# Kernel optimization log

Measured on AMD Instinct MI355X. Metric: run time of the kernel, lower is better.

The kernel has to match this reference:

```python
import jax, jax.numpy as jnp
import numpy as np

B, D, V, S = 256, 784, 128, 2  # batch, dim, max_val, n_steps
ITER_PER_CYCLE = 10
STEP_SIZES = [0.5] + [0.1] * (ITER_PER_CYCLE - 1)   # sbc: [big_step] + [small_step]*...
BAL_CONSTS = [0.9] + [0.6] * (ITER_PER_CYCLE - 1)   # sbc: [big_bal] + [small_bal]*...
TEMP = 1.0


def setup_inputs() -> dict:
    key = jax.random.key(0)
    k1, k2, k3, k4, k5 = jax.random.split(key, 5)
    x = jax.random.randint(k1, (B, D), 0, V, dtype=jnp.int32)
    W = jax.random.normal(k2, (D, D), dtype=jnp.float32) * (1.0 / D)  # keep energies moderate
    b = jax.random.normal(k3, (D,), dtype=jnp.float32) * 0.1
    # Pre-sampled Gumbel noise for the categorical proposal (one slab per inner step)
    ug = jax.random.uniform(k4, (S, B, D, V), dtype=jnp.float32, minval=1e-6, maxval=1.0 - 1e-6)
    gumbel = -jnp.log(-jnp.log(ug))
    # Uniform draws for the MH accept/reject test
    u = jax.random.uniform(k5, (S, B), dtype=jnp.float32)
    k_iter = 0
    return {"x": x, "W": W, "b": b, "gumbel": gumbel, "u": u, "k_iter": k_iter}


def reference(x, W, b, gumbel, u, k_iter):
    step_size = STEP_SIZES[k_iter % ITER_PER_CYCLE]
    bal = BAL_CONSTS[k_iter % ITER_PER_CYCLE]
    Wsym = 0.5 * (W + W.T)

    def model(xf):                      # energy: [B]
        return 0.5 * jnp.einsum('bi,bi->b', xf, xf @ Wsym) + xf @ b

    def gradf(xf):                      # d(energy)/dx: [B, D]
        return xf @ Wsym + b

    disc = jnp.arange(V, dtype=jnp.float32)[None, None, :]  # [1,1,V]

    def calc_logits(xf, g):
        # term1 - term2 from _calc_logits, fused elementwise over [B, D, V]
        diff = disc - xf[:, :, None]
        return g[:, :, None] * diff * bal - diff * diff * (0.5 / step_size)

    def body(x_cur, inp):
        g_noise, ui = inp
        xf = x_cur.astype(jnp.float32)
        g = gradf(xf)
        logits = calc_logits(xf, g)                                  # [B,D,V]
        x_delta = jnp.argmax(logits + g_noise, axis=-1)              # categorical sample [B,D]
        logp = jax.nn.log_softmax(logits, axis=-1)
        lp_forward = jnp.take_along_axis(logp, x_delta[:, :, None], axis=-1)[..., 0].sum(axis=1)
        xdf = x_delta.astype(jnp.float32)
        gd = gradf(xdf) / TEMP
        logits_d = calc_logits(xdf, gd)
        logp_d = jax.nn.log_softmax(logits_d, axis=-1)
        lp_reverse = jnp.take_along_axis(logp_d, x_cur[:, :, None], axis=-1)[..., 0].sum(axis=1)
        la = model(xdf) - model(xf) + lp_reverse - lp_forward        # log accept ratio [B]
        acc = jnp.exp(la) > ui
        x_new = jnp.where(acc[:, None], x_delta, x_cur).astype(x_cur.dtype)
        return x_new, la

    x_out, las = jax.lax.scan(body, x, (gumbel, u))
    return x_out, las[-1]
```

## Files before the change

### kernel.cpp

```cpp
#include <hip/hip_runtime.h>

#define B_ 256
#define D_ 784
#define V_ 128
#define S_ 2
#define BD (B_ * D_)
#define KSPLIT 4
#define KC 196

__device__ __forceinline__ void get_params(const int* kiter, float& ss, float& bal) {
    int k = kiter[0] % 10;
    ss  = (k == 0) ? 0.5f : 0.1f;
    bal = (k == 0) ? 0.9f : 0.6f;
}

__device__ __forceinline__ double wave_red(double v) {
#pragma unroll
    for (int o = 32; o > 0; o >>= 1) v += __shfl_down(v, o, 64);
    return v;
}

__global__ __launch_bounds__(256) void init_k(
    const float* __restrict__ W, const int* __restrict__ x,
    float* __restrict__ wsym, int* __restrict__ x_cur, float* __restrict__ xf)
{
    int gid = blockIdx.x * 256 + threadIdx.x;
    if (gid < D_ * D_) {
        int i = gid / D_, j = gid % D_;
        wsym[gid] = 0.5f * (W[gid] + W[j * D_ + i]);
    }
    if (gid < BD) {
        int xi = x[gid];
        x_cur[gid] = xi;
        xf[gid] = (float)xi;
    }
}

__global__ __launch_bounds__(256) void gemm_splitk(
    const float* __restrict__ A, const float* __restrict__ Wm,
    float* __restrict__ Cp)
{
    const int bt = blockIdx.x, dt = blockIdx.y, kz = blockIdx.z;
    const int tid = threadIdx.x;
    const int k0 = kz * KC, kend = k0 + KC;

    __shared__ float As[64][17];
    __shared__ float Ws[16][65];

    const int tx = tid & 15, ty = tid >> 4;
    const int arow = tid >> 2, ac0 = (tid & 3) * 4;
    const int wrow = tid >> 4, wc0 = (tid & 15) * 4;

    float acc[4][4] = {};

    for (int kb = k0; kb < kend; kb += 16) {
#pragma unroll
        for (int c = 0; c < 4; ++c) {
            int k = kb + ac0 + c;
            As[arow][ac0 + c] = (k < kend) ? A[(bt * 64 + arow) * D_ + k] : 0.f;
        }
#pragma unroll
        for (int c = 0; c < 4; ++c) {
            int k = kb + wrow;
            int d = dt * 64 + wc0 + c;
            Ws[wrow][wc0 + c] = (k < kend && d < D_) ? Wm[k * D_ + d] : 0.f;
        }
        __syncthreads();
#pragma unroll
        for (int kk = 0; kk < 16; ++kk) {
            float a[4], w[4];
#pragma unroll
            for (int i = 0; i < 4; ++i) a[i] = As[ty * 4 + i][kk];
#pragma unroll
            for (int j = 0; j < 4; ++j) w[j] = Ws[kk][tx * 4 + j];
#pragma unroll
            for (int i = 0; i < 4; ++i)
#pragma unroll
                for (int j = 0; j < 4; ++j)
                    acc[i][j] = fmaf(a[i], w[j], acc[i][j]);
        }
        __syncthreads();
    }

#pragma unroll
    for (int i = 0; i < 4; ++i) {
        int bb = bt * 64 + ty * 4 + i;
#pragma unroll
        for (int j = 0; j < 4; ++j) {
            int d = dt * 64 + tx * 4 + j;
            if (d < D_) Cp[(size_t)kz * BD + (size_t)bb * D_ + d] = acc[i][j];
        }
    }
}

__global__ __launch_bounds__(1024) void forward_k(
    const int* __restrict__ x_cur, const float* __restrict__ gpart,
    const float* __restrict__ bvec, const float* __restrict__ gumbel,
    const int* __restrict__ kiter, int s,
    int* __restrict__ x_delta, float* __restrict__ xdf,
    double* __restrict__ lpf, double* __restrict__ Exf)
{
    const int b = blockIdx.x, tid = threadIdx.x;
    float ss, bal; get_params(kiter, ss, bal);
    const float c2 = 0.5f / ss;

    double lp_acc = 0.0, e_acc = 0.0;

    if (tid < D_) {
        const int d = tid, bd = b * D_ + d;
        const int xi = x_cur[bd];
        const float xfv = (float)xi;

        float gv = 0.f;
#pragma unroll
        for (int p = 0; p < KSPLIT; ++p) gv += gpart[(size_t)p * BD + bd];
        gv += bvec[d];

        const float a1 = bal * gv;
        const float v0 = xfv + a1 * ss;
        int vm = (int)rintf(v0); vm = min(127, max(0, vm));
        const float dmv = v0 - (float)vm;
        const float Reff = sqrtf(30.0f / c2 + dmv * dmv);
        int lo = max(0, (int)ceilf(v0 - Reff));
        int hi = min(127, (int)floorf(v0 + Reff));
        lo = min(lo, vm); hi = max(hi, vm);

        const float dvm = (float)vm - xfv;
        const float mL = dvm * fmaf(-c2, dvm, a1);

        const float4* __restrict__ gq =
            (const float4*)(gumbel + (((size_t)s * B_ + b) * D_ + d) * V_);
        const int q0 = lo >> 2;
        float4 quad[4];
#pragma unroll
        for (int j = 0; j < 4; ++j) quad[j] = gq[min(q0 + j, 31)];

        float best = -1e30f; int imax = vm;
        float sum0 = 0.f, sum1 = 0.f;
#pragma unroll
        for (int j = 0; j < 4; ++j) {
            const int qi = q0 + j;
            const bool qok = qi < 32;
            const float qs[4] = {quad[j].x, quad[j].y, quad[j].z, quad[j].w};
#pragma unroll
            for (int c = 0; c < 4; ++c) {
                int v = 4 * qi + c;
                bool ok = qok && v >= lo && v <= hi;
                float dv = (float)v - xfv;
                float lg = dv * fmaf(-c2, dv, a1);
                float y = ok ? (lg + qs[c]) : -1e30f;
                if (y > best) { best = y; imax = v; }
                float e = expf(lg - mL);
                if (c & 1) sum1 += ok ? e : 0.f; else sum0 += ok ? e : 0.f;
            }
        }
        float lse = mL + logf(sum0 + sum1);
        float dvc = (float)imax - xfv;
        float lch = dvc * fmaf(-c2, dvc, a1);
        lp_acc = (double)(lch - lse);
        e_acc  = (double)xfv * ((double)gv + (double)bvec[d]);
        x_delta[bd] = imax;
        xdf[bd] = (float)imax;
    }

    __shared__ double wred[16];
    const int lane = tid & 63, wv = tid >> 6;
    double t = wave_red(lp_acc);
    if (lane == 0) wred[wv] = t;
    __syncthreads();
    if (tid == 0) { double sm = 0; for (int i = 0; i < 16; ++i) sm += wred[i]; lpf[b] = sm; }
    __syncthreads();
    t = wave_red(e_acc);
    if (lane == 0) wred[wv] = t;
    __syncthreads();
    if (tid == 0) { double sm = 0; for (int i = 0; i < 16; ++i) sm += wred[i]; Exf[b] = sm; }
}

__global__ __launch_bounds__(1024) void reverse_k(
    int* __restrict__ x_cur, const int* __restrict__ x_delta,
    const float* __restrict__ gpart, const float* __restrict__ bvec,
    const float* __restrict__ u, const int* __restrict__ kiter,
    int s, int last, const double* __restrict__ lpf, const double* __restrict__ Exf,
    float* __restrict__ xf_f, float* __restrict__ out)
{
    const int b = blockIdx.x, tid = threadIdx.x;
    float ss, bal; get_params(kiter, ss, bal);
    const float c2 = 0.5f / ss;

    double lp_acc = 0.0, e_acc = 0.0;

    if (tid < D_) {
        const int d = tid, bd = b * D_ + d;
        const int xi = x_cur[bd];
        const int xd = x_delta[bd];
        const float xdv = (float)xd;

        float gv = 0.f;
#pragma unroll
        for (int p = 0; p < KSPLIT; ++p) gv += gpart[(size_t)p * BD + bd];
        gv += bvec[d];

        const float a1 = bal * gv;
        const float v0 = xdv + a1 * ss;
        int vm = (int)rintf(v0); vm = min(127, max(0, vm));
        const float dmv = v0 - (float)vm;
        const float Reff = sqrtf(30.0f / c2 + dmv * dmv);
        int lo = max(0, (int)ceilf(v0 - Reff));
        int hi = min(127, (int)floorf(v0 + Reff));
        lo = min(lo, vm); hi = max(hi, vm);

        const float dvm = (float)vm - xdv;
        const float mL = dvm * fmaf(-c2, dvm, a1);
        float sum0 = 0.f, sum1 = 0.f;
#pragma unroll
        for (int j = 0; j < 16; ++j) {
            int v = lo + j;
            bool ok = v <= hi;
            float dv = (float)v - xdv;
            float lg = dv * fmaf(-c2, dv, a1);
            float e = expf(lg - mL);
            if (j & 1) sum1 += ok ? e : 0.f; else sum0 += ok ? e : 0.f;
        }
        float lse = mL + logf(sum0 + sum1);
        float dvc = (float)xi - xdv;
        float lch = dvc * fmaf(-c2, dvc, a1);
        lp_acc = (double)(lch - lse);
        e_acc  = (double)xdv * ((double)gv + (double)bvec[d]);
    }

    __shared__ double wred[16];
    __shared__ int accept_s;
    __shared__ float la_s;
    const int lane = tid & 63, wv = tid >> 6;

    double t = wave_red(lp_acc);
    if (lane == 0) wred[wv] = t;
    __syncthreads();
    double lpr = 0;
    if (tid == 0) { for (int i = 0; i < 16; ++i) lpr += wred[i]; }
    __syncthreads();
    t = wave_red(e_acc);
    if (lane == 0) wred[wv] = t;
    __syncthreads();
    if (tid == 0) {
        double exd = 0; for (int i = 0; i < 16; ++i) exd += wred[i];
        double la = 0.5 * (exd - Exf[b]) + lpr - lpf[b];
        accept_s = (exp(la) > (double)u[s * B_ + b]) ? 1 : 0;
        la_s = (float)la;
    }
    __syncthreads();

    const int acc = accept_s;
    if (tid < D_) {
        const int bd = b * D_ + tid;
        int xn = acc ? x_delta[bd] : x_cur[bd];
        x_cur[bd] = xn;
        xf_f[bd] = (float)xn;
        if (last) out[bd] = (float)xn;
    }
    if (last && tid == 0) out[BD + b] = la_s;
}

extern "C" void kernel_launch(void* const* d_in, const int* in_sizes, int n_in,
                              void* d_out, int out_size, void* d_ws, size_t ws_size,
                              hipStream_t stream)
{
    const int*   x     = (const int*)d_in[0];
    const float* W     = (const float*)d_in[1];
    const float* bv    = (const float*)d_in[2];
    const float* gum   = (const float*)d_in[3];
    const float* u     = (const float*)d_in[4];
    const int*   kiter = (const int*)d_in[5];
    float* out = (float*)d_out;

    char* w = (char*)d_ws;
    size_t off = 0;
    auto carve = [&](size_t bytes) { void* p = w + off; off += (bytes + 511) & ~511ull; return p; };
    float*  wsym    = (float*)carve((size_t)D_ * D_ * 4);
    int*    x_cur   = (int*)  carve((size_t)BD * 4);
    int*    x_delta = (int*)  carve((size_t)BD * 4);
    float*  xf      = (float*)carve((size_t)BD * 4);
    float*  xdf     = (float*)carve((size_t)BD * 4);
    float*  gpart   = (float*)carve((size_t)KSPLIT * BD * 4);
    double* lpf     = (double*)carve(B_ * 8);
    double* Exf     = (double*)carve(B_ * 8);
    (void)ws_size; (void)in_sizes; (void)n_in; (void)out_size;

    init_k<<<(D_ * D_ + 255) / 256, 256, 0, stream>>>(W, x, wsym, x_cur, xf);

    for (int s = 0; s < S_; ++s) {
        gemm_splitk<<<dim3(4, 13, KSPLIT), 256, 0, stream>>>(xf, wsym, gpart);
        forward_k<<<B_, 1024, 0, stream>>>(x_cur, gpart, bv, gum, kiter, s,
                                           x_delta, xdf, lpf, Exf);
        gemm_splitk<<<dim3(4, 13, KSPLIT), 256, 0, stream>>>(xdf, wsym, gpart);
        reverse_k<<<B_, 1024, 0, stream>>>(x_cur, x_delta, gpart, bv, u, kiter, s,
                                           (s == S_ - 1) ? 1 : 0, lpf, Exf, xf, out);
    }
}
```

Baseline: 403.1 us.

## Fuse symmetrization and int-to-float into GEMM, drop init kernel, retune split-K

Removes the init kernel by symmetrizing W on the fly inside the GEMM tile load and converting integer states to float there too, so the xf/xdf/wsym buffers disappear. Split-K is raised from 4 to 8 for more parallelism. The GEMM inner loop now uses float4 LDS reads, and the forward/reverse kernels shrink to 832 threads. The gumbel loads are clamped to the useful quad range. The cost is a transposed, strided W read per tile load, which may be uncoalesced, and twice as many partial sums to reduce.

```diff
diff --git a/kernel.cpp b/kernel.cpp
--- a/kernel.cpp
+++ b/kernel.cpp
@@ -5,8 +5,8 @@
 #define V_ 128
 #define S_ 2
 #define BD (B_ * D_)
-#define KSPLIT 4
-#define KC 196
+#define KSPLIT 8
+#define KC 98
 
 __device__ __forceinline__ void get_params(const int* kiter, float& ss, float& bal) {
     int k = kiter[0] % 10;
@@ -20,32 +20,16 @@
     return v;
 }
 
-__global__ __launch_bounds__(256) void init_k(
-    const float* __restrict__ W, const int* __restrict__ x,
-    float* __restrict__ wsym, int* __restrict__ x_cur, float* __restrict__ xf)
-{
-    int gid = blockIdx.x * 256 + threadIdx.x;
-    if (gid < D_ * D_) {
-        int i = gid / D_, j = gid % D_;
-        wsym[gid] = 0.5f * (W[gid] + W[j * D_ + i]);
-    }
-    if (gid < BD) {
-        int xi = x[gid];
-        x_cur[gid] = xi;
-        xf[gid] = (float)xi;
-    }
-}
-
 __global__ __launch_bounds__(256) void gemm_splitk(
-    const float* __restrict__ A, const float* __restrict__ Wm,
+    const int* __restrict__ Aint, const float* __restrict__ W,
     float* __restrict__ Cp)
 {
     const int bt = blockIdx.x, dt = blockIdx.y, kz = blockIdx.z;
     const int tid = threadIdx.x;
     const int k0 = kz * KC, kend = k0 + KC;
 
-    __shared__ float As[64][17];
-    __shared__ float Ws[16][65];
+    __shared__ float As[64][20];
+    __shared__ float Ws[16][68];
 
     const int tx = tid & 15, ty = tid >> 4;
     const int arow = tid >> 2, ac0 = (tid & 3) * 4;
@@ -57,27 +41,36 @@
 #pragma unroll
         for (int c = 0; c < 4; ++c) {
             int k = kb + ac0 + c;
-            As[arow][ac0 + c] = (k < kend) ? A[(bt * 64 + arow) * D_ + k] : 0.f;
+            As[arow][ac0 + c] = (k < kend) ? (float)Aint[(bt * 64 + arow) * D_ + k] : 0.f;
         }
 #pragma unroll
         for (int c = 0; c < 4; ++c) {
             int k = kb + wrow;
             int d = dt * 64 + wc0 + c;
-            Ws[wrow][wc0 + c] = (k < kend && d < D_) ? Wm[k * D_ + d] : 0.f;
+            Ws[wrow][wc0 + c] = (k < kend && d < D_)
+                ? 0.5f * (W[k * D_ + d] + W[d * D_ + k]) : 0.f;
         }
         __syncthreads();
 #pragma unroll
-        for (int kk = 0; kk < 16; ++kk) {
-            float a[4], w[4];
-#pragma unroll
-            for (int i = 0; i < 4; ++i) a[i] = As[ty * 4 + i][kk];
-#pragma unroll
-            for (int j = 0; j < 4; ++j) w[j] = Ws[kk][tx * 4 + j];
-#pragma unroll
-            for (int i = 0; i < 4; ++i)
-#pragma unroll
-                for (int j = 0; j < 4; ++j)
-                    acc[i][j] = fmaf(a[i], w[j], acc[i][j]);
+        for (int kk = 0; kk < 16; kk += 4) {
+            float va[4][4], vw[4][4];
+#pragma unroll
+            for (int i = 0; i < 4; ++i) {
+                float4 t = *(const float4*)&As[ty * 4 + i][kk];
+                va[i][0] = t.x; va[i][1] = t.y; va[i][2] = t.z; va[i][3] = t.w;
+            }
+#pragma unroll
+            for (int m = 0; m < 4; ++m) {
+                float4 t = *(const float4*)&Ws[kk + m][tx * 4];
+                vw[m][0] = t.x; vw[m][1] = t.y; vw[m][2] = t.z; vw[m][3] = t.w;
+            }
+#pragma unroll
+            for (int m = 0; m < 4; ++m)
+#pragma unroll
+                for (int i = 0; i < 4; ++i)
+#pragma unroll
+                    for (int j = 0; j < 4; ++j)
+                        acc[i][j] = fmaf(va[i][m], vw[m][j], acc[i][j]);
         }
         __syncthreads();
     }
@@ -93,12 +86,11 @@
     }
 }
 
-__global__ __launch_bounds__(1024) void forward_k(
-    const int* __restrict__ x_cur, const float* __restrict__ gpart,
+__global__ __launch_bounds__(832) void forward_k(
+    const int* __restrict__ xin, const float* __restrict__ gpart,
     const float* __restrict__ bvec, const float* __restrict__ gumbel,
     const int* __restrict__ kiter, int s,
-    int* __restrict__ x_delta, float* __restrict__ xdf,
-    double* __restrict__ lpf, double* __restrict__ Exf)
+    int* __restrict__ x_delta, double* __restrict__ lpf, double* __restrict__ Exf)
 {
     const int b = blockIdx.x, tid = threadIdx.x;
     float ss, bal; get_params(kiter, ss, bal);
@@ -108,7 +100,7 @@
 
     if (tid < D_) {
         const int d = tid, bd = b * D_ + d;
-        const int xi = x_cur[bd];
+        const int xi = xin[bd];
         const float xfv = (float)xi;
 
         float gv = 0.f;
@@ -130,17 +122,17 @@
 
         const float4* __restrict__ gq =
             (const float4*)(gumbel + (((size_t)s * B_ + b) * D_ + d) * V_);
-        const int q0 = lo >> 2;
+        const int q0 = lo >> 2, qh = hi >> 2;
         float4 quad[4];
 #pragma unroll
-        for (int j = 0; j < 4; ++j) quad[j] = gq[min(q0 + j, 31)];
+        for (int j = 0; j < 4; ++j) quad[j] = gq[min(q0 + j, qh)];
 
         float best = -1e30f; int imax = vm;
         float sum0 = 0.f, sum1 = 0.f;
 #pragma unroll
         for (int j = 0; j < 4; ++j) {
             const int qi = q0 + j;
-            const bool qok = qi < 32;
+            const bool qok = qi <= qh;
             const float qs[4] = {quad[j].x, quad[j].y, quad[j].z, quad[j].w};
 #pragma unroll
             for (int c = 0; c < 4; ++c) {
@@ -160,28 +152,28 @@
         lp_acc = (double)(lch - lse);
         e_acc  = (double)xfv * ((double)gv + (double)bvec[d]);
         x_delta[bd] = imax;
-        xdf[bd] = (float)imax;
-    }
-
-    __shared__ double wred[16];
+    }
+
+    __shared__ double wred[13];
     const int lane = tid & 63, wv = tid >> 6;
     double t = wave_red(lp_acc);
     if (lane == 0) wred[wv] = t;
     __syncthreads();
-    if (tid == 0) { double sm = 0; for (int i = 0; i < 16; ++i) sm += wred[i]; lpf[b] = sm; }
+    if (tid == 0) { double sm = 0; for (int i = 0; i < 13; ++i) sm += wred[i]; lpf[b] = sm; }
     __syncthreads();
     t = wave_red(e_acc);
     if (lane == 0) wred[wv] = t;
     __syncthreads();
-    if (tid == 0) { double sm = 0; for (int i = 0; i < 16; ++i) sm += wred[i]; Exf[b] = sm; }
-}
-
-__global__ __launch_bounds__(1024) void reverse_k(
-    int* __restrict__ x_cur, const int* __restrict__ x_delta,
+    if (tid == 0) { double sm = 0; for (int i = 0; i < 13; ++i) sm += wred[i]; Exf[b] = sm; }
+}
+
+__global__ __launch_bounds__(832) void reverse_k(
+    const int* __restrict__ xin, int* __restrict__ x_cur,
+    const int* __restrict__ x_delta,
     const float* __restrict__ gpart, const float* __restrict__ bvec,
     const float* __restrict__ u, const int* __restrict__ kiter,
     int s, int last, const double* __restrict__ lpf, const double* __restrict__ Exf,
-    float* __restrict__ xf_f, float* __restrict__ out)
+    float* __restrict__ out)
 {
     const int b = blockIdx.x, tid = threadIdx.x;
     float ss, bal; get_params(kiter, ss, bal);
@@ -191,7 +183,7 @@
 
     if (tid < D_) {
         const int d = tid, bd = b * D_ + d;
-        const int xi = x_cur[bd];
+        const int xi = xin[bd];
         const int xd = x_delta[bd];
         const float xdv = (float)xd;
 
@@ -228,7 +220,7 @@
         e_acc  = (double)xdv * ((double)gv + (double)bvec[d]);
     }
 
-    __shared__ double wred[16];
+    __shared__ double wred[13];
     __shared__ int accept_s;
     __shared__ float la_s;
     const int lane = tid & 63, wv = tid >> 6;
@@ -237,13 +229,13 @@
     if (lane == 0) wred[wv] = t;
     __syncthreads();
     double lpr = 0;
-    if (tid == 0) { for (int i = 0; i < 16; ++i) lpr += wred[i]; }
+    if (tid == 0) { for (int i = 0; i < 13; ++i) lpr += wred[i]; }
     __syncthreads();
     t = wave_red(e_acc);
     if (lane == 0) wred[wv] = t;
     __syncthreads();
     if (tid == 0) {
-        double exd = 0; for (int i = 0; i < 16; ++i) exd += wred[i];
+        double exd = 0; for (int i = 0; i < 13; ++i) exd += wred[i];
         double la = 0.5 * (exd - Exf[b]) + lpr - lpf[b];
         accept_s = (exp(la) > (double)u[s * B_ + b]) ? 1 : 0;
         la_s = (float)la;
@@ -253,9 +245,8 @@
     const int acc = accept_s;
     if (tid < D_) {
         const int bd = b * D_ + tid;
-        int xn = acc ? x_delta[bd] : x_cur[bd];
+        int xn = acc ? x_delta[bd] : xin[bd];
         x_cur[bd] = xn;
-        xf_f[bd] = (float)xn;
         if (last) out[bd] = (float)xn;
     }
     if (last && tid == 0) out[BD + b] = la_s;
@@ -276,24 +267,20 @@
     char* w = (char*)d_ws;
     size_t off = 0;
     auto carve = [&](size_t bytes) { void* p = w + off; off += (bytes + 511) & ~511ull; return p; };
-    float*  wsym    = (float*)carve((size_t)D_ * D_ * 4);
-    int*    x_cur   = (int*)  carve((size_t)BD * 4);
-    int*    x_delta = (int*)  carve((size_t)BD * 4);
-    float*  xf      = (float*)carve((size_t)BD * 4);
-    float*  xdf     = (float*)carve((size_t)BD * 4);
-    float*  gpart   = (float*)carve((size_t)KSPLIT * BD * 4);
+    int*    x_cur   = (int*)   carve((size_t)BD * 4);
+    int*    x_delta = (int*)   carve((size_t)BD * 4);
+    float*  gpart   = (float*) carve((size_t)KSPLIT * BD * 4);
     double* lpf     = (double*)carve(B_ * 8);
     double* Exf     = (double*)carve(B_ * 8);
     (void)ws_size; (void)in_sizes; (void)n_in; (void)out_size;
 
-    init_k<<<(D_ * D_ + 255) / 256, 256, 0, stream>>>(W, x, wsym, x_cur, xf);
-
     for (int s = 0; s < S_; ++s) {
-        gemm_splitk<<<dim3(4, 13, KSPLIT), 256, 0, stream>>>(xf, wsym, gpart);
-        forward_k<<<B_, 1024, 0, stream>>>(x_cur, gpart, bv, gum, kiter, s,
-                                           x_delta, xdf, lpf, Exf);
-        gemm_splitk<<<dim3(4, 13, KSPLIT), 256, 0, stream>>>(xdf, wsym, gpart);
-        reverse_k<<<B_, 1024, 0, stream>>>(x_cur, x_delta, gpart, bv, u, kiter, s,
-                                           (s == S_ - 1) ? 1 : 0, lpf, Exf, xf, out);
-    }
-}
+        const int* xin = (s == 0) ? x : x_cur;
+        gemm_splitk<<<dim3(4, 13, KSPLIT), 256, 0, stream>>>(xin, W, gpart);
+        forward_k<<<B_, 832, 0, stream>>>(xin, gpart, bv, gum, kiter, s,
+                                          x_delta, lpf, Exf);
+        gemm_splitk<<<dim3(4, 13, KSPLIT), 256, 0, stream>>>(x_delta, W, gpart);
+        reverse_k<<<B_, 832, 0, stream>>>(xin, x_cur, x_delta, gpart, bv, u, kiter, s,
+                                          (s == S_ - 1) ? 1 : 0, lpf, Exf, out);
+    }
+}
```

After: 383.8 us. -4.8%, faster.
